# Optimization experiments

Hardware: AMD Instinct MI355X
Metric: run time of the kernel (lower is better)

Reference implementation:

```python
import jax, jax.numpy as jnp
import numpy as np

D_MODEL, D_STATE, D_CONV, EXPAND = 512, 16, 4, 2
D_INNER = D_MODEL * EXPAND
BATCH, LENGTH = 2, 2048

def setup_inputs() -> dict:
    key = jax.random.key(0)
    ks = jax.random.split(key, 12)
    def lecun(k, shape, fan_in):
        return jax.random.normal(k, shape, jnp.float32) * (1.0 / np.sqrt(fan_in))
    x = jax.random.normal(ks[0], (BATCH, LENGTH, D_MODEL), jnp.float32)
    w_in = lecun(ks[1], (D_MODEL, 2 * D_INNER), D_MODEL)
    conv_k = lecun(ks[2], (D_CONV, D_INNER, D_INNER), D_CONV * D_INNER)  # (L_k, in, out)
    conv_b = jnp.zeros((D_INNER,), jnp.float32)
    w_delta = lecun(ks[3], (D_INNER, D_INNER), D_INNER)
    b_delta = jnp.zeros((D_INNER,), jnp.float32)
    w_B = lecun(ks[4], (D_INNER, D_STATE), D_INNER)
    b_B = jnp.zeros((D_STATE,), jnp.float32)
    w_C = lecun(ks[5], (D_INNER, D_STATE), D_INNER)
    b_C = jnp.zeros((D_STATE,), jnp.float32)
    A = lecun(ks[6], (D_INNER, D_STATE), D_INNER)  # dead param in original (deltaA unused)
    w_out = lecun(ks[7], (D_INNER, D_MODEL), D_INNER)
    return {"x": x, "w_in": w_in, "conv_k": conv_k, "conv_b": conv_b,
            "w_delta": w_delta, "b_delta": b_delta, "w_B": w_B, "b_B": b_B,
            "w_C": w_C, "b_C": b_C, "A": A, "w_out": w_out}

def reference(x, w_in, conv_k, conv_b, w_delta, b_delta, w_B, b_B, w_C, b_C, A, w_out):
    batch, length, _ = x.shape
    # input projection and gate split
    x_proj = x @ w_in                                   # (B, L, 2*d_inner)
    x_z, z = jnp.split(x_proj, 2, axis=-1)              # each (B, L, d_inner)
    # depthwise-style SAME conv over L (flax nn.Conv: full conv, kernel (Lk, in, out))
    x_conv = jax.lax.conv_general_dilated(
        x_z, conv_k, window_strides=(1,), padding='SAME',
        dimension_numbers=('NLC', 'LIO', 'NLC')) + conv_b
    x_conv = jax.nn.silu(x_conv)                        # (B, L, d_inner)
    delta = jax.nn.softplus(x_conv @ w_delta + b_delta)  # (B, L, d_inner)
    Bm = x_conv @ w_B + b_B                             # (B, L, d_state)
    Cm = x_conv @ w_C + b_C                             # (B, L, d_state)
    # NOTE: original computes deltaA = exp(delta * -exp(A)) but never uses it (dead code).
    deltaB_x = delta[..., None] * Bm[..., None, :] * x_conv[..., :, None]  # (B,L,d_inner,d_state)
    decay = jnp.cumprod(jnp.full((length,), 0.95, x.dtype))  # 0.95^(t+1)
    hidden = jnp.cumsum(deltaB_x * decay[None, :, None, None], axis=1)
    y = jnp.einsum('blns,bls->bln', hidden, Cm)         # (B, L, d_inner)
    y = y * jax.nn.silu(z)
    return y @ w_out                                    # (B, L, d_model)
```

## Files before the change

kernel.cpp:

```cpp
#include <hip/hip_runtime.h>
#include <hip/hip_bf16.h>
#include <math.h>

#define DMODEL 512
#define DINNER 1024
#define DSTATE 16
#define SEQLEN 2048
#define NTOK   4096
#define CHUNK  64
#define NCHUNK (SEQLEN / CHUNK)

typedef __bf16 bf16x8 __attribute__((ext_vector_type(8)));
typedef float  f32x4  __attribute__((ext_vector_type(4)));

__device__ __forceinline__ float silu_f(float x) {
    return x / (1.0f + __expf(-x));
}

__device__ __forceinline__ float softplus_f(float x) {
    return fmaxf(x, 0.f) + __logf(1.0f + __expf(-fabsf(x)));
}

__device__ __forceinline__ int swz(int r, int s) {
    return r * 64 + ((s ^ (r & 7)) << 3);
}

__device__ __forceinline__ void gload16(const void* g, void* l) {
    __builtin_amdgcn_global_load_lds(
        (const __attribute__((address_space(1))) void*)g,
        (__attribute__((address_space(3))) void*)l, 16, 0, 0);
}

__device__ __forceinline__ void cvt4(const float* src, __hip_bfloat16* dst) {
    float4 v = *reinterpret_cast<const float4*>(src);
    __hip_bfloat16 tmp[4] = {__float2bfloat16(v.x), __float2bfloat16(v.y),
                             __float2bfloat16(v.z), __float2bfloat16(v.w)};
    *reinterpret_cast<ushort4*>(dst) = *reinterpret_cast<const ushort4*>(tmp);
}

template<int MODE, int TBM, int TBN>
__global__ __launch_bounds__(256)
void mgemm(const __hip_bfloat16* __restrict__ A, int lda,
           const __hip_bfloat16* __restrict__ WT, int ldw,
           float* __restrict__ C0, __hip_bfloat16* __restrict__ Cb,
           __hip_bfloat16* __restrict__ Czb, int ldc,
           int K, const float* __restrict__ bias,
           const __hip_bfloat16* __restrict__ xc,
           const __hip_bfloat16* __restrict__ WT2, int ldw2,
           const __hip_bfloat16* __restrict__ zpage,
           const float* __restrict__ bB, const float* __restrict__ bC,
           float* __restrict__ BmO, float* __restrict__ CmO,
           __hip_bfloat16* __restrict__ Pb1)
{
    constexpr int MI = TBM / 32;
    constexpr int MJ = TBN / 32;
    __shared__ __align__(16) __hip_bfloat16 As[TBM * 64];
    __shared__ __align__(16) __hip_bfloat16 Bs[TBN * 64];

    const int nb  = gridDim.x * gridDim.y;
    const int lin = blockIdx.y * gridDim.x + blockIdx.x;
    const int cpx = nb >> 3;
    const int sl  = (lin & 7) * cpx + (lin >> 3);
    const int bm  = (sl / gridDim.x) * TBM;
    const int bn  = (sl % gridDim.x) * TBN;

    if (MODE == 4) { A += blockIdx.z * 1024; Cb += blockIdx.z * 512; }

    const int  xsel = (MODE == 0) ? (bn >> 10) : 0;
    const bool zblk = (MODE == 0) && (xsel == 2);
    const int  bnb  = (MODE == 0) ? (bn & 1023) : bn;
    const __hip_bfloat16* Wp = zblk ? WT2 : WT;
    const int  ldwp = zblk ? ldw2 : ldw;
    const int  Keff = (MODE == 0 && zblk) ? DMODEL : K;
    const int  koff = (MODE == 0 && xsel == 1) ? 1024 : 0;

    const int tid  = threadIdx.x;
    const int wid  = tid >> 6, lane = tid & 63;
    const int wr   = (wid >> 1) * (TBM / 2), wc = (wid & 1) * (TBN / 2);
    const int llo  = lane & 15, lhi = lane >> 4;

    f32x4 acc[MI][MJ] = {};

    const int srow0 = wid * 8 + (lane >> 3);
    const int sphys = lane & 7;

    auto stage_tile = [&](int k0) {
#pragma unroll
        for (int q2 = 0; q2 < MI; ++q2) {
            int row  = q2 * 32 + srow0;
            int sdat = sphys ^ (row & 7);
            const __hip_bfloat16* srcA;
            if (MODE == 0 && !zblk) {
                int kg  = koff + k0;
                int kid = kg >> 9;
                int gr  = bm + row;
                int l2  = (gr & (SEQLEN - 1)) + kid - 1;
                srcA = ((unsigned)l2 < (unsigned)SEQLEN)
                     ? A + (size_t)(gr + kid - 1) * lda + (kg & 511) + sdat * 8
                     : zpage;
            } else {
                srcA = A + (size_t)(bm + row) * lda + k0 + sdat * 8;
            }
            gload16(srcA, &As[q2 * 2048 + wid * 512]);
        }
#pragma unroll
        for (int q2 = 0; q2 < MJ; ++q2) {
            int row  = q2 * 32 + srow0;
            int sdat = sphys ^ (row & 7);
            gload16(Wp + (size_t)(bnb + row) * ldwp + koff + k0 + sdat * 8,
                    &Bs[q2 * 2048 + wid * 512]);
        }
    };

    const int NT = Keff / 64;
    for (int t = 0; t < NT; ++t) {
        stage_tile(t * 64);
        __syncthreads();
#pragma unroll
        for (int kk = 0; kk < 2; ++kk) {
            bf16x8 af[MI], bv[MJ];
#pragma unroll
            for (int i = 0; i < MI; ++i)
                af[i] = *reinterpret_cast<const bf16x8*>(&As[swz(wr + i * 16 + llo, kk * 4 + lhi)]);
#pragma unroll
            for (int j = 0; j < MJ; ++j)
                bv[j] = *reinterpret_cast<const bf16x8*>(&Bs[swz(wc + j * 16 + llo, kk * 4 + lhi)]);
#pragma unroll
            for (int i = 0; i < MI; ++i)
#pragma unroll
                for (int j = 0; j < MJ; ++j)
                    acc[i][j] = __builtin_amdgcn_mfma_f32_16x16x32_bf16(af[i], bv[j], acc[i][j], 0, 0, 0);
        }
        __syncthreads();
    }

#pragma unroll
    for (int i = 0; i < MI; ++i) {
#pragma unroll
        for (int q2 = 0; q2 < 4; ++q2) {
            int m = bm + wr + i * 16 + lhi * 4 + q2;
            float dec = 1.0f;
            if (MODE == 2)
                dec = __expf((float)((m & (SEQLEN - 1)) + 1) * -0.051293294f);
#pragma unroll
            for (int j = 0; j < MJ; ++j) {
                int nrel = wc + j * 16 + llo;
                int n = bn + nrel;
                float v = acc[i][j][q2];
                if (MODE == 0) {
                    int col = bnb + nrel;
                    if (zblk) {
                        Czb[(size_t)m * DINNER + col] = __float2bfloat16(v);
                    } else {
                        __hip_bfloat16* P = xsel ? Pb1 : Cb;
                        P[(size_t)m * DINNER + col] = __float2bfloat16(v);
                    }
                } else if (MODE == 2) {
                    if (n < DINNER) {
                        float sp = softplus_f(v + bias[n]);
                        float xcv = __bfloat162float(xc[(size_t)m * DINNER + n]);
                        Cb[(size_t)m * DINNER + n] = __float2bfloat16(sp * xcv * dec);
                    } else {
                        int col = n - DINNER;
                        if (col < 16)
                            BmO[(size_t)m * DSTATE + col] = v + bB[col];
                        else if (col < 32)
                            CmO[(size_t)m * DSTATE + (col - 16)] = v + bC[col - 16];
                    }
                } else if (MODE == 4) {
                    Cb[(size_t)m * ldc + n] = __float2bfloat16(v);
                } else {
                    C0[(size_t)m * ldc + n] = v;
                }
            }
        }
    }
}

__global__ __launch_bounds__(256)
void combine_k(const __hip_bfloat16* __restrict__ P0,
               const __hip_bfloat16* __restrict__ P1,
               const float* __restrict__ bias,
               __hip_bfloat16* __restrict__ xcb)
{
    int idx = blockIdx.x * 256 + threadIdx.x;
    size_t off = (size_t)idx * 4;
    int n = (int)(off & 1023);
    ushort4 a = *reinterpret_cast<const ushort4*>(&P0[off]);
    ushort4 b = *reinterpret_cast<const ushort4*>(&P1[off]);
    __hip_bfloat16 o[4];
#pragma unroll
    for (int j = 0; j < 4; ++j) {
        float va = __bfloat162float(((const __hip_bfloat16*)&a)[j]);
        float vb = __bfloat162float(((const __hip_bfloat16*)&b)[j]);
        o[j] = __float2bfloat16(silu_f(va + vb + bias[n + j]));
    }
    *reinterpret_cast<ushort4*>(&xcb[off]) = *reinterpret_cast<const ushort4*>(o);
}

__global__ __launch_bounds__(256)
void prep_k(const float* __restrict__ x, const float* __restrict__ w_in,
            const float* __restrict__ conv_k, const float* __restrict__ w_del,
            const float* __restrict__ w_B, const float* __restrict__ w_C,
            const float* __restrict__ w_out,
            __hip_bfloat16* __restrict__ xb, __hip_bfloat16* __restrict__ W1b,
            __hip_bfloat16* __restrict__ w2T, __hip_bfloat16* __restrict__ convT,
            __hip_bfloat16* __restrict__ wdelT, __hip_bfloat16* __restrict__ woutT,
            __hip_bfloat16* __restrict__ zpage)
{
    __shared__ float t[32][33];
    const int b = blockIdx.x, tid = threadIdx.x;
    if (b < 2048) {
        int idx = b * 256 + tid;
        int r = idx >> 7, c = (idx & 127) * 4;
        cvt4(x + (size_t)r * DMODEL + c, xb + (size_t)r * DMODEL + c);
    } else if (b < 2560) {
        int idx = (b - 2048) * 256 + tid;
        int r = idx >> 8, c = (idx & 255) * 4;
        cvt4(w_in + (size_t)r * (2 * DINNER) + c, W1b + (size_t)r * DINNER + c);
    } else if (b < 8704) {
        const float* in; __hip_bfloat16* outp; int R, ldin, ntx, local;
        if (b < 3072)      { local = b - 2560; in = w_in + DINNER; outp = w2T;   R = 512;  ldin = 2048; ntx = 32; }
        else if (b < 7168) { local = b - 3072; in = conv_k;        outp = convT; R = 4096; ldin = 1024; ntx = 32; }
        else if (b < 8192) { local = b - 7168; in = w_del;         outp = wdelT; R = 1024; ldin = 1024; ntx = 32; }
        else               { local = b - 8192; in = w_out;         outp = woutT; R = 1024; ldin = 512;  ntx = 16; }
        int bx = (local % ntx) * 32, by = (local / ntx) * 32;
        int tx = tid & 31, ty = tid >> 5;
#pragma unroll
        for (int q = 0; q < 4; ++q)
            t[ty + q * 8][tx] = in[(size_t)(by + ty + q * 8) * ldin + bx + tx];
        __syncthreads();
#pragma unroll
        for (int q = 0; q < 4; ++q)
            outp[(size_t)(bx + ty + q * 8) * R + by + tx] = __float2bfloat16(t[tx][ty + q * 8]);
    } else if (b < 8832) {
        int idx = (b - 8704) * 256 + tid;
        int sel = idx >> 14;
        int rem = idx & 16383;
        int s = rem >> 10, k = rem & 1023;
        const float* src = sel ? w_C : w_B;
        wdelT[(size_t)(1024 + sel * 16 + s) * DINNER + k] =
            __float2bfloat16(src[(size_t)k * DSTATE + s]);
    } else {
        int local = b - 8832;
        ushort4 zero = {0, 0, 0, 0};
        if (local < 8) {
            int idx = local * 256 + tid;
            *reinterpret_cast<ushort4*>(&zpage[idx * 4]) = zero;
        } else {
            int idx = (local - 8) * 256 + tid;
            *reinterpret_cast<ushort4*>(&wdelT[(size_t)1056 * DINNER + idx * 4]) = zero;
        }
    }
}

__global__ __launch_bounds__(256)
void chunkS_k(const __hip_bfloat16* __restrict__ wb, const float* __restrict__ Bm,
              float* __restrict__ S)
{
    constexpr int LDW = 72;
    __shared__ __align__(16) __hip_bfloat16 wT[128 * LDW];
    __shared__ __align__(16) __hip_bfloat16 bT[16 * 80];
    const int bc = blockIdx.x, n0 = blockIdx.y * 128, t0 = bc * CHUNK;
    const int tid = threadIdx.x;
#pragma unroll
    for (int q = 0; q < 8; ++q) {
        int idx = tid + q * 256;
        int t = idx >> 5, n4 = (idx & 31) * 4;
        int key = ((n4 >> 2) & 7) << 3;
        int tx = t ^ key;
        ushort4 v = *reinterpret_cast<const ushort4*>(
            &wb[(size_t)(t0 + t) * DINNER + n0 + n4]);
        wT[(n4 + 0) * LDW + tx] = *(const __hip_bfloat16*)&v.x;
        wT[(n4 + 1) * LDW + tx] = *(const __hip_bfloat16*)&v.y;
        wT[(n4 + 2) * LDW + tx] = *(const __hip_bfloat16*)&v.z;
        wT[(n4 + 3) * LDW + tx] = *(const __hip_bfloat16*)&v.w;
    }
#pragma unroll
    for (int q = 0; q < 4; ++q) {
        int idx = tid + q * 256;
        int t = idx >> 4, s = idx & 15;
        bT[s * 80 + t] = __float2bfloat16(Bm[(size_t)(t0 + t) * DSTATE + s]);
    }
    __syncthreads();
    const int wid = tid >> 6, lane = tid & 63;
    const int llo = lane & 15, lhi = lane >> 4;
    f32x4 acc[2] = {};
#pragma unroll
    for (int kk = 0; kk < 2; ++kk) {
        bf16x8 bv = *reinterpret_cast<const bf16x8*>(&bT[llo * 80 + kk * 32 + lhi * 8]);
#pragma unroll
        for (int i = 0; i < 2; ++i) {
            int r = wid * 32 + i * 16 + llo;
            int kbase = (kk * 32 + lhi * 8) ^ (((r >> 2) & 7) << 3);
            bf16x8 af = *reinterpret_cast<const bf16x8*>(&wT[r * LDW + kbase]);
            acc[i] = __builtin_amdgcn_mfma_f32_16x16x32_bf16(af, bv, acc[i], 0, 0, 0);
        }
    }
#pragma unroll
    for (int i = 0; i < 2; ++i)
#pragma unroll
        for (int q = 0; q < 4; ++q) {
            int n = wid * 32 + i * 16 + lhi * 4 + q;
            S[((size_t)bc * DINNER + n0 + n) * DSTATE + llo] = acc[i][q];
        }
}

__global__ __launch_bounds__(256)
void hpre_k(const float* __restrict__ S, __hip_bfloat16* __restrict__ Hb)
{
    int idx = blockIdx.x * 256 + threadIdx.x;
    int b  = idx >> 14;
    int ns = idx & 16383;
    float acc = 0.f;
    for (int c = 0; c < NCHUNK; ++c) {
        size_t off = ((size_t)(b * NCHUNK + c)) * (DINNER * DSTATE) + ns;
        Hb[off] = __float2bfloat16(acc);
        acc += S[off];
    }
}

__global__ __launch_bounds__(256)
void intra_k(const __hip_bfloat16* __restrict__ wb,
             const float* __restrict__ Bm, const float* __restrict__ Cm,
             const __hip_bfloat16* __restrict__ Hb,
             const __hip_bfloat16* __restrict__ zb,
             __hip_bfloat16* __restrict__ gb)
{
    constexpr int LDP  = 104;
    constexpr int LDC  = 40;
    __shared__ __align__(16) __hip_bfloat16 csb[64 * LDC];
    __shared__ __align__(16) __hip_bfloat16 bsb[64 * LDC];
    __shared__ __align__(16) __hip_bfloat16 Pb [64 * LDP];
    __shared__ __align__(16) __hip_bfloat16 Wb [64 * LDP];

    const int bc = blockIdx.x;
    const int n0 = blockIdx.y * 64;
    const int t0 = bc * CHUNK;
    const int tid = threadIdx.x;
    const int wid = tid >> 6, lane = tid & 63;
    const int llo = lane & 15, lhi = lane >> 4;
    const int wr = (wid >> 1) * 32, wc = (wid & 1) * 32;
    const __hip_bfloat16 z16 = __float2bfloat16(0.f);

#pragma unroll
    for (int q = 0; q < 4; ++q) {
        int idx = tid + q * 256;
        int j = idx >> 4, s = idx & 15;
        __hip_bfloat16 cb = __float2bfloat16(Cm[(size_t)(t0 + j) * DSTATE + s]);
        csb[j * LDC + s]      = cb;
        csb[j * LDC + 16 + s] = z16;
        bsb[j * LDC + s]      = __float2bfloat16(Bm[(size_t)(t0 + j) * DSTATE + s]);
        bsb[j * LDC + 16 + s] = z16;
        Pb[j * LDP + 64 + s]  = cb;
        Pb[j * LDP + 80 + s]  = z16;
        Wb[j * LDP + 64 + s]  = Hb[((size_t)bc * DINNER + n0 + j) * DSTATE + s];
        Wb[j * LDP + 80 + s]  = z16;
    }
#pragma unroll
    for (int q = 0; q < 4; ++q) {
        int c = tid + q * 256;
        int t = c >> 4, c4 = (c & 15) * 4;
        ushort4 v = *reinterpret_cast<const ushort4*>(
            &wb[(size_t)(t0 + t) * DINNER + n0 + c4]);
        Wb[(c4 + 0) * LDP + t] = *(const __hip_bfloat16*)&v.x;
        Wb[(c4 + 1) * LDP + t] = *(const __hip_bfloat16*)&v.y;
        Wb[(c4 + 2) * LDP + t] = *(const __hip_bfloat16*)&v.z;
        Wb[(c4 + 3) * LDP + t] = *(const __hip_bfloat16*)&v.w;
    }
    __syncthreads();

    {
        f32x4 pacc[2][2] = {};
        bf16x8 ap[2], bp[2];
#pragma unroll
        for (int i = 0; i < 2; ++i)
            ap[i] = *reinterpret_cast<const bf16x8*>(&csb[(wr + i * 16 + llo) * LDC + lhi * 8]);
#pragma unroll
        for (int j = 0; j < 2; ++j)
            bp[j] = *reinterpret_cast<const bf16x8*>(&bsb[(wc + j * 16 + llo) * LDC + lhi * 8]);
#pragma unroll
        for (int i = 0; i < 2; ++i)
#pragma unroll
            for (int j = 0; j < 2; ++j)
                pacc[i][j] = __builtin_amdgcn_mfma_f32_16x16x32_bf16(ap[i], bp[j], pacc[i][j], 0, 0, 0);
#pragma unroll
        for (int i = 0; i < 2; ++i)
#pragma unroll
            for (int q = 0; q < 4; ++q) {
                int l = wr + i * 16 + lhi * 4 + q;
#pragma unroll
                for (int j = 0; j < 2; ++j) {
                    int t = wc + j * 16 + llo;
                    float pv = (t <= l) ? pacc[i][j][q] : 0.f;
                    Pb[l * LDP + t] = __float2bfloat16(pv);
                }
            }
    }
    __syncthreads();

    f32x4 yacc[2][2] = {};
#pragma unroll
    for (int k0 = 0; k0 < 3; ++k0) {
        bf16x8 af[2], bv[2];
#pragma unroll
        for (int i = 0; i < 2; ++i)
            af[i] = *reinterpret_cast<const bf16x8*>(&Pb[(wr + i * 16 + llo) * LDP + k0 * 32 + lhi * 8]);
#pragma unroll
        for (int j = 0; j < 2; ++j)
            bv[j] = *reinterpret_cast<const bf16x8*>(&Wb[(wc + j * 16 + llo) * LDP + k0 * 32 + lhi * 8]);
#pragma unroll
        for (int i = 0; i < 2; ++i)
#pragma unroll
            for (int j = 0; j < 2; ++j)
                yacc[i][j] = __builtin_amdgcn_mfma_f32_16x16x32_bf16(af[i], bv[j], yacc[i][j], 0, 0, 0);
    }

#pragma unroll
    for (int i = 0; i < 2; ++i)
#pragma unroll
        for (int q = 0; q < 4; ++q) {
            int l = wr + i * 16 + lhi * 4 + q;
            int token = t0 + l;
#pragma unroll
            for (int j = 0; j < 2; ++j) {
                int n = wc + j * 16 + llo;
                float z = __bfloat162float(zb[(size_t)token * DINNER + n0 + n]);
                gb[(size_t)token * DINNER + n0 + n] =
                    __float2bfloat16(yacc[i][j][q] * silu_f(z));
            }
        }
}

extern "C" void kernel_launch(void* const* d_in, const int* in_sizes, int n_in,
                              void* d_out, int out_size, void* d_ws, size_t ws_size,
                              hipStream_t stream) {
    const float* x      = (const float*)d_in[0];
    const float* w_in   = (const float*)d_in[1];
    const float* conv_k = (const float*)d_in[2];
    const float* conv_b = (const float*)d_in[3];
    const float* w_del  = (const float*)d_in[4];
    const float* b_del  = (const float*)d_in[5];
    const float* w_B    = (const float*)d_in[6];
    const float* b_B    = (const float*)d_in[7];
    const float* w_C    = (const float*)d_in[8];
    const float* b_C    = (const float*)d_in[9];
    const float* w_out  = (const float*)d_in[11];
    float* out = (float*)d_out;

    float* Bm    = (float*)d_ws;
    float* Cm    = Bm + (size_t)NTOK * DSTATE;
    float* S     = Cm + (size_t)NTOK * DSTATE;
    __hip_bfloat16* Hb    = (__hip_bfloat16*)(S + (size_t)2 * NCHUNK * DINNER * DSTATE);
    __hip_bfloat16* xb    = Hb    + (size_t)2 * NCHUNK * DINNER * DSTATE;
    __hip_bfloat16* xcb   = xb    + (size_t)NTOK * DMODEL;
    __hip_bfloat16* zb    = xcb   + (size_t)NTOK * DINNER;
    __hip_bfloat16* gb    = zb    + (size_t)NTOK * DINNER;
    __hip_bfloat16* wbufb = gb    + (size_t)NTOK * DINNER;
    __hip_bfloat16* W1b   = wbufb + (size_t)NTOK * DINNER;
    __hip_bfloat16* w2T   = W1b   + (size_t)DMODEL * DINNER;
    __hip_bfloat16* convT = w2T   + (size_t)DINNER * DMODEL;
    __hip_bfloat16* wdelT = convT + (size_t)4 * DINNER * DINNER;
    __hip_bfloat16* woutT = wdelT + (size_t)1088 * DINNER;
    __hip_bfloat16* FT    = woutT + (size_t)DINNER * DMODEL;
    __hip_bfloat16* zpage = FT    + (size_t)DINNER * 2048;
    __hip_bfloat16* P0    = zpage + 8192;
    __hip_bfloat16* P1    = P0    + (size_t)NTOK * DINNER;

    prep_k<<<8872, 256, 0, stream>>>(x, w_in, conv_k, w_del, w_B, w_C, w_out,
                                     xb, W1b, w2T, convT, wdelT, woutT, zpage);

    mgemm<4, 64, 64><<<dim3(DMODEL / 64, DINNER / 64, 4), 256, 0, stream>>>(
        convT, 4 * DINNER, W1b, DINNER, nullptr, FT, nullptr, 4 * DMODEL, DINNER,
        nullptr, nullptr, nullptr, 0, zpage, nullptr, nullptr, nullptr, nullptr, nullptr);
    mgemm<0, 64, 64><<<dim3(48, NTOK / 64), 256, 0, stream>>>(
        xb, DMODEL, FT, 4 * DMODEL, nullptr, P0, zb, DINNER, 1024,
        nullptr, nullptr, w2T, DMODEL, zpage, nullptr, nullptr, nullptr, nullptr, P1);
    combine_k<<<NTOK * DINNER / 1024, 256, 0, stream>>>(P0, P1, conv_b, xcb);
    mgemm<2, 64, 64><<<dim3(1088 / 64, NTOK / 64), 256, 0, stream>>>(
        xcb, DINNER, wdelT, DINNER, nullptr, wbufb, nullptr, DINNER, DINNER,
        b_del, xcb, nullptr, 0, zpage, b_B, b_C, Bm, Cm, nullptr);
    chunkS_k<<<dim3(2 * NCHUNK, DINNER / 128), 256, 0, stream>>>(wbufb, Bm, S);
    hpre_k<<<dim3(2 * DINNER * DSTATE / 256), 256, 0, stream>>>(S, Hb);
    intra_k<<<dim3(2 * NCHUNK, DINNER / 64), 256, 0, stream>>>(wbufb, Bm, Cm, Hb, zb, gb);
    mgemm<3, 64, 32><<<dim3(DMODEL / 32, NTOK / 64), 256, 0, stream>>>(
        gb, DINNER, woutT, DINNER, out, nullptr, nullptr, DMODEL, DINNER,
        nullptr, nullptr, nullptr, 0, zpage, nullptr, nullptr, nullptr, nullptr, nullptr);
}
```

Before: 115.1 us.

## Double-buffer GEMM LDS tiles with async prefetch and enlarge input-projection tile

Adds a two-stage LDS ping-pong to the shared GEMM template. The next K-tile's global_load_lds is issued before computing on the current tile, with explicit vmcnt waits and raw s_barrier replacing __syncthreads. This aims to hide global load latency behind MFMA work. Separately, the input-projection GEMM uses 128-row tiles instead of 64, halving its grid in the M dimension; this doubles LDS use and could reduce occupancy.

```diff
diff --git a/kernel.cpp b/kernel.cpp
--- a/kernel.cpp
+++ b/kernel.cpp
@@ -29,6 +29,16 @@
     __builtin_amdgcn_global_load_lds(
         (const __attribute__((address_space(1))) void*)g,
         (__attribute__((address_space(3))) void*)l, 16, 0, 0);
+}
+
+template<int N>
+__device__ __forceinline__ void waitcnt_vm() {
+    if constexpr (N == 0)      asm volatile("s_waitcnt vmcnt(0)" ::: "memory");
+    else if constexpr (N == 3) asm volatile("s_waitcnt vmcnt(3)" ::: "memory");
+    else if constexpr (N == 4) asm volatile("s_waitcnt vmcnt(4)" ::: "memory");
+    else if constexpr (N == 6) asm volatile("s_waitcnt vmcnt(6)" ::: "memory");
+    else                       asm volatile("s_waitcnt vmcnt(0)" ::: "memory");
+    __builtin_amdgcn_sched_barrier(0);
 }
 
 __device__ __forceinline__ void cvt4(const float* src, __hip_bfloat16* dst) {
@@ -54,8 +64,9 @@
 {
     constexpr int MI = TBM / 32;
     constexpr int MJ = TBN / 32;
-    __shared__ __align__(16) __hip_bfloat16 As[TBM * 64];
-    __shared__ __align__(16) __hip_bfloat16 Bs[TBN * 64];
+    constexpr int NLD = MI + MJ;
+    __shared__ __align__(16) __hip_bfloat16 As[2 * TBM * 64];
+    __shared__ __align__(16) __hip_bfloat16 Bs[2 * TBN * 64];
 
     const int nb  = gridDim.x * gridDim.y;
     const int lin = blockIdx.y * gridDim.x + blockIdx.x;
@@ -84,7 +95,9 @@
     const int srow0 = wid * 8 + (lane >> 3);
     const int sphys = lane & 7;
 
-    auto stage_tile = [&](int k0) {
+    auto stage_tile = [&](int k0, int buf) {
+        __hip_bfloat16* Ad = As + buf * (TBM * 64);
+        __hip_bfloat16* Bd = Bs + buf * (TBN * 64);
 #pragma unroll
         for (int q2 = 0; q2 < MI; ++q2) {
             int row  = q2 * 32 + srow0;
@@ -101,37 +114,47 @@
             } else {
                 srcA = A + (size_t)(bm + row) * lda + k0 + sdat * 8;
             }
-            gload16(srcA, &As[q2 * 2048 + wid * 512]);
+            gload16(srcA, &Ad[q2 * 2048 + wid * 512]);
         }
 #pragma unroll
         for (int q2 = 0; q2 < MJ; ++q2) {
             int row  = q2 * 32 + srow0;
             int sdat = sphys ^ (row & 7);
             gload16(Wp + (size_t)(bnb + row) * ldwp + koff + k0 + sdat * 8,
-                    &Bs[q2 * 2048 + wid * 512]);
+                    &Bd[q2 * 2048 + wid * 512]);
         }
     };
 
     const int NT = Keff / 64;
+    stage_tile(0, 0);
     for (int t = 0; t < NT; ++t) {
-        stage_tile(t * 64);
-        __syncthreads();
+        if (t + 1 < NT) {
+            stage_tile((t + 1) * 64, (t + 1) & 1);
+            waitcnt_vm<NLD>();
+        } else {
+            waitcnt_vm<0>();
+        }
+        __builtin_amdgcn_s_barrier();
+        const __hip_bfloat16* Ab = As + (t & 1) * (TBM * 64);
+        const __hip_bfloat16* Bb = Bs + (t & 1) * (TBN * 64);
 #pragma unroll
         for (int kk = 0; kk < 2; ++kk) {
             bf16x8 af[MI], bv[MJ];
 #pragma unroll
             for (int i = 0; i < MI; ++i)
-                af[i] = *reinterpret_cast<const bf16x8*>(&As[swz(wr + i * 16 + llo, kk * 4 + lhi)]);
+                af[i] = *reinterpret_cast<const bf16x8*>(&Ab[swz(wr + i * 16 + llo, kk * 4 + lhi)]);
 #pragma unroll
             for (int j = 0; j < MJ; ++j)
-                bv[j] = *reinterpret_cast<const bf16x8*>(&Bs[swz(wc + j * 16 + llo, kk * 4 + lhi)]);
+                bv[j] = *reinterpret_cast<const bf16x8*>(&Bb[swz(wc + j * 16 + llo, kk * 4 + lhi)]);
 #pragma unroll
             for (int i = 0; i < MI; ++i)
 #pragma unroll
                 for (int j = 0; j < MJ; ++j)
                     acc[i][j] = __builtin_amdgcn_mfma_f32_16x16x32_bf16(af[i], bv[j], acc[i][j], 0, 0, 0);
         }
-        __syncthreads();
+        asm volatile("s_waitcnt lgkmcnt(0)" ::: "memory");
+        __builtin_amdgcn_sched_barrier(0);
+        __builtin_amdgcn_s_barrier();
     }
 
 #pragma unroll
@@ -473,7 +496,7 @@
     mgemm<4, 64, 64><<<dim3(DMODEL / 64, DINNER / 64, 4), 256, 0, stream>>>(
         convT, 4 * DINNER, W1b, DINNER, nullptr, FT, nullptr, 4 * DMODEL, DINNER,
         nullptr, nullptr, nullptr, 0, zpage, nullptr, nullptr, nullptr, nullptr, nullptr);
-    mgemm<0, 64, 64><<<dim3(48, NTOK / 64), 256, 0, stream>>>(
+    mgemm<0, 128, 64><<<dim3(48, NTOK / 128), 256, 0, stream>>>(
         xb, DMODEL, FT, 4 * DMODEL, nullptr, P0, zb, DINNER, 1024,
         nullptr, nullptr, w2T, DMODEL, zpage, nullptr, nullptr, nullptr, nullptr, P1);
     combine_k<<<NTOK * DINNER / 1024, 256, 0, stream>>>(P0, P1, conv_b, xcb);
```

Result: slower. 124.7 us (+8.3%).
